# Kernel optimization log

Measured on AMD Instinct MI355X. Metric: run time of the kernel, lower is better.

## Reference

```python
import jax, jax.numpy as jnp
import numpy as np

VP = 0.4
EP = 0.21

def _c_matrix():
    # Faithfully replicate the original Ci (including its asymmetric rows 2) and invert.
    Ci = np.zeros((6, 6), dtype=np.float64)
    Ci[0, 0] = 1 / EP; Ci[0, 1] = -VP / EP; Ci[0, 2] = -VP / EP
    Ci[1, 0] = -VP / EP; Ci[1, 1] = 1 / EP; Ci[1, 2] = -VP / EP
    Ci[2, 0] = -VP;      Ci[2, 1] = -VP;      Ci[2, 2] = 1 / EP
    Ci[3, 3] = 2 * (1 + VP) / EP
    Ci[4, 4] = 2 * (1 + VP) / EP
    Ci[5, 5] = 2 * (1 + VP) / EP
    return np.linalg.inv(Ci).astype(np.float32)

C_MAT = jnp.asarray(_c_matrix())
N = 12288

def setup_inputs() -> dict:
    key = jax.random.key(0)
    k1, k2, k3 = jax.random.split(key, 3)
    xyz = jax.random.normal(k1, (N, 3), dtype=jnp.float32)
    new_xyz = jax.random.normal(k2, (N, 3), dtype=jnp.float32)
    # ~half the points are 'inside' (gt_sdf < 1e-8)
    gt_sdf = jax.random.uniform(k3, (N,), dtype=jnp.float32) - 0.5
    return {"new_xyz": new_xyz, "xyz": xyz, "gt_sdf": gt_sdf}

def reference(new_xyz, xyz, gt_sdf):
    motion = new_xyz - xyz                      # [N,3]
    inside = gt_sdf < 1e-8                      # [N] bool, selects inside points
    w = new_xyz                                 # warped coordinates (KNN space)
    n = w.shape[0]
    # Brute-force NN among inside points (KDTree k=2, second neighbor == nearest non-self).
    sq = jnp.sum(w * w, axis=1)                 # [N]
    d2 = sq[:, None] + sq[None, :] - 2.0 * (w @ w.T)   # [N,N] squared distances
    BIG = jnp.float32(1e30)
    bad_col = (~inside)[None, :] | jnp.eye(n, dtype=bool)
    d2 = jnp.where(bad_col, BIG, d2)
    nn_idx = jnp.argmin(d2, axis=1)             # nearest inside neighbor (excluding self)
    nn_d = jnp.sqrt(jnp.maximum(jnp.min(d2, axis=1), 0.0))
    # tree_list1 filter: drop rows whose nearest neighbor is a duplicate point
    valid = inside & (nn_d > 1e-8)              # [N]
    dm = motion[nn_idx] - motion                # motion_delta
    dc = w[nn_idx] - w + 1e-8                   # cords_delta (+1e-8 as in original)
    v = valid[:, None]
    dm = jnp.where(v, dm, 0.0)                  # neutralize masked rows (keep shapes static)
    dc = jnp.where(v, dc, 1.0)
    du, dv, dw = dm[:, 0], dm[:, 1], dm[:, 2]
    dx, dy, dz = dc[:, 0], dc[:, 1], dc[:, 2]
    et = jnp.stack([du / dx, dv / dy, dw / dz,
                    (du / dy + dv / dx) / 2,
                    (du / dz + dw / dx) / 2,
                    (dw / dy + dv / dz) / 2], axis=1)   # [N,6] strain tensor
    # diag(et @ C @ et.T) as an O(N) batched quadratic form
    q = jnp.einsum('ni,ij,nj->n', et, C_MAT, et)
    q = jnp.where(valid, q, 0.0)
    n_valid = jnp.sum(valid).astype(jnp.float32)
    return jnp.linalg.norm(q) / n_valid
```

## Files before the change

### kernel.cpp

```cpp
#include <hip/hip_runtime.h>
#include <math.h>
#include <string.h>

#define N 12288
#define QP 7168
#define TILE 128
#define NSPLIT 56
#define ACCS 2
#define QBLK 512
#define NQB 14
#define BT 1024
#define RPT (N / BT)
#define NPART (QP / 256)

typedef unsigned long long ull;

struct CMat { float c[6][6]; };

__global__ __launch_bounds__(1024) void build_kernel(
    const float* __restrict__ new_xyz,
    const float* __restrict__ gt_sdf,
    float4* __restrict__ pts,
    int* __restrict__ cj,
    int* __restrict__ Mout,
    ull* __restrict__ best,
    unsigned int* __restrict__ ticket)
{
    const int tid = threadIdx.x;
    const int lane = tid & 63;
    const int wave = tid >> 6;

    float px[RPT], py[RPT], pz[RPT];
    unsigned flags = 0;

    #pragma unroll
    for (int r = 0; r < RPT; ++r) {
        const int idx = r * BT + tid;
        px[r] = new_xyz[3 * idx + 0];
        py[r] = new_xyz[3 * idx + 1];
        pz[r] = new_xyz[3 * idx + 2];
        if (gt_sdf[idx] < 1e-8f) flags |= (1u << r);
    }

    __shared__ int scnt[RPT * 16];
    __shared__ int spref[RPT * 16 + 1];

    #pragma unroll
    for (int r = 0; r < RPT; ++r) {
        const ull m = __ballot((flags >> r) & 1u);
        if (lane == 0) scnt[r * 16 + wave] = __popcll(m);
    }
    __syncthreads();

    if (tid < RPT * 16) {
        int p = 0;
        for (int f = 0; f < tid; ++f) p += scnt[f];
        spref[tid] = p;
        if (tid == RPT * 16 - 1) spref[RPT * 16] = p + scnt[tid];
    }
    __syncthreads();

    const int M = spref[RPT * 16];

    #pragma unroll
    for (int r = 0; r < RPT; ++r) {
        const ull m = __ballot((flags >> r) & 1u);
        const int rank = __popcll(m & ((1ull << lane) - 1ull));
        const int slot = spref[r * 16 + wave] + rank;
        if (((flags >> r) & 1u) && slot < QP) {
            pts[slot] = make_float4(-2.0f * px[r], -2.0f * py[r], -2.0f * pz[r],
                                    px[r] * px[r] + py[r] * py[r] + pz[r] * pz[r]);
            cj[slot] = r * BT + tid;
        }
    }

    if (tid == 0) { *Mout = M; *ticket = 0u; }
    for (int s = M + tid; s < QP; s += BT) {
        pts[s] = make_float4(0.0f, 0.0f, 0.0f, 3e30f);
        cj[s] = 0;
    }
    for (int s = tid; s < QP; s += BT) best[s] = ~0ull;
}

template<bool CAREFUL>
__device__ __forceinline__ void nn_inner(
    const float4* __restrict__ tile,
    const float* wx, const float* wy, const float* wz,
    const int* kx,
    float* bd, int* bk)
{
    #pragma unroll 8
    for (int k = 0; k < TILE; ++k) {
        const float4 b = tile[k];
        #pragma unroll
        for (int a = 0; a < ACCS; ++a) {
            float t = fmaf(wz[a], b.z, b.w);
            t = fmaf(wy[a], b.y, t);
            t = fmaf(wx[a], b.x, t);
            bool ok = t < bd[a];
            if (CAREFUL) ok = ok && (k != kx[a]);
            if (ok) { bd[a] = t; bk[a] = k; }
        }
    }
}

__global__ __launch_bounds__(256, 4) void nn_kernel(
    const float4* __restrict__ pts,
    const int* __restrict__ Mptr,
    ull* __restrict__ best)
{
    const int tid = threadIdx.x;
    const int qbase = blockIdx.x * QBLK;
    const int s = blockIdx.y;
    const int jb = s * TILE;

    const int M = *Mptr;
    if (jb >= M || qbase >= M) return;

    float wx[ACCS], wy[ACCS], wz[ACCS];
    int kx[ACCS];
    #pragma unroll
    for (int a = 0; a < ACCS; ++a) {
        const int ci = qbase + tid + a * 256;
        const float4 q = pts[ci];
        wx[a] = -0.5f * q.x;
        wy[a] = -0.5f * q.y;
        wz[a] = -0.5f * q.z;
        kx[a] = ci - jb;
    }

    __shared__ float4 tile[TILE];
    if (tid < TILE) tile[tid] = pts[jb + tid];
    __syncthreads();

    float bd[ACCS];
    int bk[ACCS];
    #pragma unroll
    for (int a = 0; a < ACCS; ++a) { bd[a] = 3.0e38f; bk[a] = 0; }

    const bool dirty = (jb < qbase + QBLK) && (jb + TILE > qbase);
    if (dirty)
        nn_inner<true>(tile, wx, wy, wz, kx, bd, bk);
    else
        nn_inner<false>(tile, wx, wy, wz, kx, bd, bk);

    #pragma unroll
    for (int a = 0; a < ACCS; ++a) {
        const int ci = qbase + tid + a * 256;
        unsigned u = __float_as_uint(bd[a]);
        u = ((int)u < 0) ? ~u : (u | 0x80000000u);
        const ull v = ((ull)u << 32) | (ull)(unsigned)(jb + bk[a]);
        atomicMin(&best[ci], v);
    }
}

__global__ __launch_bounds__(256) void loss_kernel(
    const float* __restrict__ new_xyz,
    const float* __restrict__ xyz,
    const int* __restrict__ cj,
    const int* __restrict__ Mptr,
    const ull* __restrict__ best_arr,
    double* __restrict__ partial_sum,
    unsigned int* __restrict__ partial_cnt,
    unsigned int* __restrict__ ticket,
    float* __restrict__ out,
    CMat C)
{
    const int tid = threadIdx.x;
    const int ci = blockIdx.x * 256 + tid;

    const ull best = best_arr[ci];
    const int M = *Mptr;
    const bool real = (ci < M);

    const unsigned u = (unsigned)(best >> 32);
    const unsigned bits = (u & 0x80000000u) ? (u ^ 0x80000000u) : ~u;
    const float key = __uint_as_float(bits);
    const int cc = real ? (int)(unsigned)(best & 0xffffffffu) : 0;

    const int i  = real ? cj[ci] : 0;
    const int nn = cj[cc];

    const float wix = new_xyz[3 * i + 0];
    const float wiy = new_xyz[3 * i + 1];
    const float wiz = new_xyz[3 * i + 2];
    const float sqi = wix * wix + wiy * wiy + wiz * wiz;

    const float d2 = sqi + key;
    const float nnd = sqrtf(fmaxf(d2, 0.0f));
    const bool valid = real && (nnd > 1e-8f);

    float q = 0.0f;
    if (valid) {
        const float xix = xyz[3 * i + 0], xiy = xyz[3 * i + 1], xiz = xyz[3 * i + 2];
        const float wnx = new_xyz[3 * nn + 0], wny = new_xyz[3 * nn + 1], wnz = new_xyz[3 * nn + 2];
        const float xnx = xyz[3 * nn + 0],     xny = xyz[3 * nn + 1],     xnz = xyz[3 * nn + 2];

        const float du = (wnx - xnx) - (wix - xix);
        const float dv = (wny - xny) - (wiy - xiy);
        const float dw = (wnz - xnz) - (wiz - xiz);
        const float dx = wnx - wix + 1e-8f;
        const float dy = wny - wiy + 1e-8f;
        const float dz = wnz - wiz + 1e-8f;

        float et[6];
        et[0] = du / dx;
        et[1] = dv / dy;
        et[2] = dw / dz;
        et[3] = (du / dy + dv / dx) * 0.5f;
        et[4] = (du / dz + dw / dx) * 0.5f;
        et[5] = (dw / dy + dv / dz) * 0.5f;

        #pragma unroll
        for (int a = 0; a < 6; ++a) {
            float s2 = 0.0f;
            #pragma unroll
            for (int b2 = 0; b2 < 6; ++b2) s2 += C.c[a][b2] * et[b2];
            q += et[a] * s2;
        }
    }

    double q2 = (double)q * (double)q;
    #pragma unroll
    for (int off = 32; off > 0; off >>= 1)
        q2 += __shfl_down(q2, off, 64);
    const ull vm = __ballot(valid);
    const int lane = tid & 63;
    const int wid = tid >> 6;

    __shared__ double wsum[4];
    __shared__ unsigned wcnt2[4];
    __shared__ bool sdone;
    if (lane == 0) { wsum[wid] = q2; wcnt2[wid] = (unsigned)__popcll(vm); }
    __syncthreads();
    if (tid == 0) {
        partial_sum[blockIdx.x] = wsum[0] + wsum[1] + wsum[2] + wsum[3];
        partial_cnt[blockIdx.x] = wcnt2[0] + wcnt2[1] + wcnt2[2] + wcnt2[3];
        __threadfence();
        const unsigned t = atomicAdd(ticket, 1u);
        sdone = (t == NPART - 1);
    }
    __syncthreads();

    if (sdone && tid < 64) {
        __threadfence();
        double s = (tid < NPART) ? partial_sum[tid] : 0.0;
        double c = (tid < NPART) ? (double)partial_cnt[tid] : 0.0;
        #pragma unroll
        for (int off = 32; off > 0; off >>= 1) {
            s += __shfl_down(s, off, 64);
            c += __shfl_down(c, off, 64);
        }
        if (tid == 0) out[0] = (float)(sqrt(s) / c);
    }
}

static void build_cmat(CMat* M)
{
    const double VP = 0.4, EP = 0.21;
    double A[6][12];
    memset(A, 0, sizeof(A));
    double Ci[6][6];
    memset(Ci, 0, sizeof(Ci));
    Ci[0][0] = 1.0 / EP; Ci[0][1] = -VP / EP; Ci[0][2] = -VP / EP;
    Ci[1][0] = -VP / EP; Ci[1][1] = 1.0 / EP; Ci[1][2] = -VP / EP;
    Ci[2][0] = -VP;      Ci[2][1] = -VP;      Ci[2][2] = 1.0 / EP;
    Ci[3][3] = 2.0 * (1.0 + VP) / EP;
    Ci[4][4] = Ci[3][3];
    Ci[5][5] = Ci[3][3];

    for (int i = 0; i < 6; ++i) {
        for (int j = 0; j < 6; ++j) A[i][j] = Ci[i][j];
        A[i][6 + i] = 1.0;
    }
    for (int col = 0; col < 6; ++col) {
        int piv = col;
        for (int r = col + 1; r < 6; ++r)
            if (fabs(A[r][col]) > fabs(A[piv][col])) piv = r;
        if (piv != col)
            for (int c = 0; c < 12; ++c) { double t = A[col][c]; A[col][c] = A[piv][c]; A[piv][c] = t; }
        const double d = A[col][col];
        for (int c = 0; c < 12; ++c) A[col][c] /= d;
        for (int r = 0; r < 6; ++r) {
            if (r == col) continue;
            const double f = A[r][col];
            if (f == 0.0) continue;
            for (int c = 0; c < 12; ++c) A[r][c] -= f * A[col][c];
        }
    }
    for (int i = 0; i < 6; ++i)
        for (int j = 0; j < 6; ++j)
            M->c[i][j] = (float)A[i][6 + j];
}

extern "C" void kernel_launch(void* const* d_in, const int* in_sizes, int n_in,
                              void* d_out, int out_size, void* d_ws, size_t ws_size,
                              hipStream_t stream)
{
    const float* new_xyz = (const float*)d_in[0];
    const float* xyz     = (const float*)d_in[1];
    const float* gt_sdf  = (const float*)d_in[2];
    float* out = (float*)d_out;

    char* p = (char*)d_ws;
    float4* pts = (float4*)p;                    p += (size_t)QP * 16;
    int* cj = (int*)p;                           p += (size_t)QP * 4;
    int* Mptr = (int*)p;                         p += 16;
    ull* best = (ull*)p;                         p += (size_t)QP * 8;
    double* partial_sum = (double*)p;            p += NPART * sizeof(double);
    unsigned int* partial_cnt = (unsigned int*)p; p += NPART * sizeof(unsigned int);
    unsigned int* ticket = (unsigned int*)p;

    CMat C;
    build_cmat(&C);

    build_kernel<<<1, BT, 0, stream>>>(new_xyz, gt_sdf, pts, cj, Mptr, best, ticket);
    nn_kernel<<<dim3(NQB, NSPLIT), 256, 0, stream>>>(pts, Mptr, best);
    loss_kernel<<<QP / 256, 256, 0, stream>>>(new_xyz, xyz, cj, Mptr, best,
                                              partial_sum, partial_cnt, ticket,
                                              out, C);
}
```

Baseline: 80.39 us.

## Parallelize point compaction across twelve blocks with redundant prefix counts

The build kernel that compacts inside points used to run as a single 1024-thread block looping over all points. It now launches one block per 1024-point chunk. Each block recomputes the count of inside points in earlier chunks to find its output offset, so the order stays stable. The aim is to shorten this serial front stage before the NN kernel, at the cost of redundant gt_sdf reads. The padding entries of cj are no longer zeroed.

```diff
diff --git a/kernel.cpp b/kernel.cpp
--- a/kernel.cpp
+++ b/kernel.cpp
@@ -10,7 +10,7 @@
 #define QBLK 512
 #define NQB 14
 #define BT 1024
-#define RPT (N / BT)
+#define BB 12
 #define NPART (QP / 256)
 
 typedef unsigned long long ull;
@@ -27,59 +27,60 @@
     unsigned int* __restrict__ ticket)
 {
     const int tid = threadIdx.x;
+    const int b = blockIdx.x;
     const int lane = tid & 63;
     const int wave = tid >> 6;
 
-    float px[RPT], py[RPT], pz[RPT];
-    unsigned flags = 0;
-
-    #pragma unroll
-    for (int r = 0; r < RPT; ++r) {
-        const int idx = r * BT + tid;
-        px[r] = new_xyz[3 * idx + 0];
-        py[r] = new_xyz[3 * idx + 1];
-        pz[r] = new_xyz[3 * idx + 2];
-        if (gt_sdf[idx] < 1e-8f) flags |= (1u << r);
-    }
-
-    __shared__ int scnt[RPT * 16];
-    __shared__ int spref[RPT * 16 + 1];
-
-    #pragma unroll
-    for (int r = 0; r < RPT; ++r) {
-        const ull m = __ballot((flags >> r) & 1u);
-        if (lane == 0) scnt[r * 16 + wave] = __popcll(m);
-    }
-    __syncthreads();
-
-    if (tid < RPT * 16) {
-        int p = 0;
-        for (int f = 0; f < tid; ++f) p += scnt[f];
-        spref[tid] = p;
-        if (tid == RPT * 16 - 1) spref[RPT * 16] = p + scnt[tid];
-    }
-    __syncthreads();
-
-    const int M = spref[RPT * 16];
-
-    #pragma unroll
-    for (int r = 0; r < RPT; ++r) {
-        const ull m = __ballot((flags >> r) & 1u);
-        const int rank = __popcll(m & ((1ull << lane) - 1ull));
-        const int slot = spref[r * 16 + wave] + rank;
-        if (((flags >> r) & 1u) && slot < QP) {
-            pts[slot] = make_float4(-2.0f * px[r], -2.0f * py[r], -2.0f * pz[r],
-                                    px[r] * px[r] + py[r] * py[r] + pz[r] * pz[r]);
-            cj[slot] = r * BT + tid;
-        }
-    }
-
-    if (tid == 0) { *Mout = M; *ticket = 0u; }
-    for (int s = M + tid; s < QP; s += BT) {
-        pts[s] = make_float4(0.0f, 0.0f, 0.0f, 3e30f);
-        cj[s] = 0;
-    }
-    for (int s = tid; s < QP; s += BT) best[s] = ~0ull;
+    int cpre = 0;
+    #pragma unroll
+    for (int r = 0; r < BB - 1; ++r) {
+        const float sv = (r < b) ? gt_sdf[r * BT + tid] : 1.0f;
+        cpre += (sv < 1e-8f) ? 1 : 0;
+    }
+    #pragma unroll
+    for (int off = 32; off > 0; off >>= 1)
+        cpre += __shfl_down(cpre, off, 64);
+
+    const int idx = b * BT + tid;
+    const float px = new_xyz[3 * idx + 0];
+    const float py = new_xyz[3 * idx + 1];
+    const float pz = new_xyz[3 * idx + 2];
+    const bool ins = gt_sdf[idx] < 1e-8f;
+    const ull m = __ballot(ins);
+    const int rank = __popcll(m & ((1ull << lane) - 1ull));
+
+    __shared__ int wpre[16];
+    __shared__ int wcnt[16];
+    __shared__ int woff[16];
+    __shared__ int tot_s;
+    if (lane == 0) { wpre[wave] = cpre; wcnt[wave] = __popcll(m); }
+    __syncthreads();
+    if (tid == 0) {
+        int cb = 0;
+        for (int w = 0; w < 16; ++w) cb += wpre[w];
+        int run = cb;
+        for (int w = 0; w < 16; ++w) { woff[w] = run; run += wcnt[w]; }
+        tot_s = run;
+    }
+    __syncthreads();
+
+    const int slot = woff[wave] + rank;
+    if (ins && slot < QP) {
+        pts[slot] = make_float4(-2.0f * px, -2.0f * py, -2.0f * pz,
+                                px * px + py * py + pz * pz);
+        cj[slot] = idx;
+    }
+
+    const int gid = b * BT + tid;
+    if (gid < QP) best[gid] = ~0ull;
+    if (gid == 0) *ticket = 0u;
+
+    if (b == BB - 1) {
+        const int M = tot_s;
+        if (tid == 0) *Mout = M;
+        for (int s = M + tid; s < QP; s += BT)
+            pts[s] = make_float4(0.0f, 0.0f, 0.0f, 3e30f);
+    }
 }
 
 template<bool CAREFUL>
@@ -314,7 +315,7 @@
     CMat C;
     build_cmat(&C);
 
-    build_kernel<<<1, BT, 0, stream>>>(new_xyz, gt_sdf, pts, cj, Mptr, best, ticket);
+    build_kernel<<<BB, BT, 0, stream>>>(new_xyz, gt_sdf, pts, cj, Mptr, best, ticket);
     nn_kernel<<<dim3(NQB, NSPLIT), 256, 0, stream>>>(pts, Mptr, best);
     loss_kernel<<<QP / 256, 256, 0, stream>>>(new_xyz, xyz, cj, Mptr, best,
                                               partial_sum, partial_cnt, ticket,
```

Result: faster. 76.95 us, median of 2 (-4.3%).
